# Performance work log

Hardware: AMD Instinct MI355X
Metric: run time of the kernel (lower is better)

## Reference

```python
import jax, jax.numpy as jnp
import numpy as np

B, S, H = 2, 2048, 1024
NH, HD = 16, 64  # num heads, head dim


def setup_inputs() -> dict:
    key = jax.random.key(0)
    ks = jax.random.split(key, 8)
    scale = 0.02
    return {
        "hidden_states": jax.random.normal(ks[0], (B, S, H), dtype=jnp.float32),
        "attention_mask": jnp.zeros((B, 1, 1, S), dtype=jnp.float32),
        "Wq": jax.random.normal(ks[1], (H, H), dtype=jnp.float32) * scale,
        "bq": jnp.zeros((H,), dtype=jnp.float32),
        "Wk": jax.random.normal(ks[2], (H, H), dtype=jnp.float32) * scale,
        "bk": jnp.zeros((H,), dtype=jnp.float32),
        "Wv": jax.random.normal(ks[3], (H, H), dtype=jnp.float32) * scale,
        "bv": jnp.zeros((H,), dtype=jnp.float32),
    }


def _split_heads(x):
    # [B,S,H] -> [B,NH,S,HD]
    b, s, _ = x.shape
    return x.reshape(b, s, NH, HD).transpose(0, 2, 1, 3)


def reference(hidden_states, attention_mask, Wq, bq, Wk, bk, Wv, bv):
    q = _split_heads(hidden_states @ Wq.T + bq)
    k = _split_heads(hidden_states @ Wk.T + bk)
    v = _split_heads(hidden_states @ Wv.T + bv)
    # scores: [B,NH,S,S]
    scores = jnp.einsum("bhqd,bhkd->bhqk", q, k) / jnp.sqrt(jnp.float32(HD))
    scores = scores + attention_mask
    att = jax.nn.softmax(scores, axis=-1)  # dropout is identity in eval
    ctx = jnp.einsum("bhqk,bhkd->bhqd", att, v)
    # [B,NH,S,HD] -> [B,S,H]
    return ctx.transpose(0, 2, 1, 3).reshape(hidden_states.shape[0], hidden_states.shape[1], NH * HD)
```

## Files before the change

kernel.cpp:

```cpp
#include <hip/hip_runtime.h>
#include <stdint.h>

#define BB 2
#define SS 2048
#define HH 1024
#define NH 16
#define HD 64

#define LOG2E 1.4426950408889634f
#define QSCALE (0.125f * LOG2E)

typedef short bfrag  __attribute__((ext_vector_type(8)));
typedef short bfrag4 __attribute__((ext_vector_type(4)));
typedef float f32x4  __attribute__((ext_vector_type(4)));

__device__ __forceinline__ short f2bf(float f) {
    union { float f; uint32_t u; } v; v.f = f;
    uint32_t r = (v.u + 0x7fffu + ((v.u >> 16) & 1u)) >> 16;
    return (short)r;
}

__global__ __launch_bounds__(256) void cvt_all(
    const float* __restrict__ X,  const float* __restrict__ Wq,
    const float* __restrict__ Wk, const float* __restrict__ Wv,
    const float* __restrict__ mask,
    short* __restrict__ Xb, short* __restrict__ Wcat,
    float* __restrict__ maskl)
{
    int i = blockIdx.x * 256 + threadIdx.x;
    if (i >= 1835008) {
        int off = i - 1835008;
        float4 f = ((const float4*)mask)[off];
        f.x *= LOG2E; f.y *= LOG2E; f.z *= LOG2E; f.w *= LOG2E;
        ((float4*)maskl)[off] = f;
        return;
    }
    const float* src; short* dst; int off;
    if (i < 1048576)      { src = X;  dst = Xb;                 off = i; }
    else if (i < 1310720) { src = Wq; dst = Wcat;               off = i - 1048576; }
    else if (i < 1572864) { src = Wk; dst = Wcat + 1048576;     off = i - 1310720; }
    else                  { src = Wv; dst = Wcat + 2097152;     off = i - 1572864; }
    float4 f = ((const float4*)src)[off];
    short4 s;
    s.x = f2bf(f.x); s.y = f2bf(f.y); s.z = f2bf(f.z); s.w = f2bf(f.w);
    ((short4*)dst)[off] = s;
}

__device__ __forceinline__ void gload_lds16(const void* g, void* lds) {
    __builtin_amdgcn_global_load_lds(
        (__attribute__((address_space(1))) void*)(uintptr_t)g,
        (__attribute__((address_space(3))) void*)(uintptr_t)lds,
        16, 0, 0);
}

__global__ __launch_bounds__(256, 3) void qkv_gemm(
    const short* __restrict__ X, const short* __restrict__ Wcat,
    const float* __restrict__ bq, const float* __restrict__ bk, const float* __restrict__ bv,
    short* __restrict__ Qo, short* __restrict__ Ko, short* __restrict__ Vo)
{
    __shared__ __align__(16) short smem[17408];

    const int tid  = threadIdx.x;
    const int wave = tid >> 6, lane = tid & 63;
    const int quad = lane >> 4, l15 = lane & 15;
    const int mTile = blockIdx.y * 128;
    const int nTile = blockIdx.x * 128;
    const int z = nTile >> 10;
    const int nLocT = nTile & 1023;
    const float* bias = (z == 0) ? bq : (z == 1) ? bk : bv;

    f32x4 acc[4][4];
#pragma unroll
    for (int i = 0; i < 4; ++i)
#pragma unroll
        for (int j = 0; j < 4; ++j) acc[i][j] = (f32x4)0.0f;

    const int srow  = lane >> 3;
    const int c_lin = lane & 7;
    const int mBase = (wave >> 1) * 64;
    const int nBase = (wave & 1) * 64;

    for (int k0 = 0; k0 < 1024; k0 += 64) {
        __syncthreads();
#pragma unroll
        for (int i = 0; i < 4; ++i) {
            int row = i * 32 + wave * 8 + srow;
            int cg  = c_lin ^ (row & 7);
            gload_lds16(X + (size_t)(mTile + row) * 1024 + k0 + cg * 8,
                        (char*)smem + i * 4096 + wave * 1024);
            gload_lds16(Wcat + (size_t)(nTile + row) * 1024 + k0 + cg * 8,
                        (char*)smem + 16384 + i * 4096 + wave * 1024);
        }
        __syncthreads();

#pragma unroll
        for (int kt = 0; kt < 2; ++kt) {
            bfrag af[4], bf[4];
#pragma unroll
            for (int t = 0; t < 4; ++t) {
                int arow = mBase + t * 16 + l15;
                int aslot = (kt * 4 + quad) ^ (arow & 7);
                af[t] = *(const bfrag*)((const char*)smem + arow * 128 + aslot * 16);
                int brow = nBase + t * 16 + l15;
                int bslot = (kt * 4 + quad) ^ (brow & 7);
                bf[t] = *(const bfrag*)((const char*)smem + 16384 + brow * 128 + bslot * 16);
            }
#pragma unroll
            for (int mt = 0; mt < 4; ++mt)
#pragma unroll
                for (int ct = 0; ct < 4; ++ct)
                    acc[mt][ct] = __builtin_amdgcn_mfma_f32_16x16x32_bf16(
                        af[mt], bf[ct], acc[mt][ct], 0, 0, 0);
        }
    }

    __syncthreads();
    const int b = mTile >> 11, sBase = mTile & 2047;

    if (z == 2) {
#pragma unroll
        for (int mt = 0; mt < 4; ++mt)
#pragma unroll
            for (int ct = 0; ct < 4; ++ct)
#pragma unroll
                for (int r = 0; r < 4; ++r) {
                    int nl = nBase + ct * 16 + l15;
                    int sl = mBase + mt * 16 + quad * 4 + r;
                    smem[nl * 136 + sl] = f2bf(acc[mt][ct][r] + bias[nLocT + nl]);
                }
        __syncthreads();
#pragma unroll
        for (int p = 0; p < 8; ++p) {
            int nl = p * 16 + (tid >> 4);
            int c  = tid & 15;
            bfrag v8 = *(const bfrag*)(smem + nl * 136 + c * 8);
            int ng = nLocT + nl, hh = ng >> 6, d = ng & 63;
            *(bfrag*)(Vo + ((size_t)(b * 16 + hh) * 64 + d) * 2048 + sBase + c * 8) = v8;
        }
    } else {
        short* Out = (z == 0) ? Qo : Ko;
        float scale = (z == 0) ? QSCALE : 1.0f;
#pragma unroll
        for (int mt = 0; mt < 4; ++mt)
#pragma unroll
            for (int ct = 0; ct < 4; ++ct)
#pragma unroll
                for (int r = 0; r < 4; ++r) {
                    int ml = mBase + mt * 16 + quad * 4 + r;
                    int nl = nBase + ct * 16 + l15;
                    smem[ml * 136 + nl] = f2bf((acc[mt][ct][r] + bias[nLocT + nl]) * scale);
                }
        __syncthreads();
#pragma unroll
        for (int p = 0; p < 8; ++p) {
            int ml = p * 16 + (tid >> 4);
            int c  = tid & 15;
            bfrag v8 = *(const bfrag*)(smem + ml * 136 + c * 8);
            int s  = sBase + ml;
            int nl = nLocT + c * 8, hh = nl >> 6, d = nl & 63;
            *(bfrag*)(Out + (((size_t)(b * 16 + hh) << 11) + s) * 64 + d) = v8;
        }
    }
}

__global__ __launch_bounds__(256, 4) void attn_kernel(
    const short* __restrict__ Qb, const short* __restrict__ Kb, const short* __restrict__ Vb,
    const float* __restrict__ maskl, float* __restrict__ out)
{
    __shared__ __align__(16) char smem[32768];

    const int tid  = threadIdx.x;
    const int wave = tid >> 6, lane = tid & 63;
    const int quad = lane >> 4, l15 = lane & 15;
    const int bh = blockIdx.y, b = bh >> 4, h = bh & 15;
    const int qBase = blockIdx.x * 64 + wave * 16;

    int ksrc[2], vsrc[2];
#pragma unroll
    for (int i = 0; i < 2; ++i) {
        int ci = wave * 128 + i * 64 + lane;
        int r = ci >> 3, c = ci & 7;
        int cs = (c ^ (r & 7)) * 16;
        ksrc[i] = r * 128  + cs;
        vsrc[i] = r * 4096 + cs;
    }
    const char* kPtr = (const char*)(Kb + (size_t)bh * SS * HD);
    const char* vPtr = (const char*)(Vb + (size_t)bh * HD * SS);
    const char* mSrc = (const char*)(maskl + b * SS) + quad * 16;

    const short* Qp = Qb + ((size_t)bh * SS + qBase) * HD;
    bfrag qf[2];
#pragma unroll
    for (int kt = 0; kt < 2; ++kt)
        qf[kt] = *(const bfrag*)(Qp + (size_t)l15 * HD + kt * 32 + quad * 8);

    int kAddr[2];
#pragma unroll
    for (int kt = 0; kt < 2; ++kt)
        kAddr[kt] = l15 * 128 + (((kt * 4 + quad) ^ (l15 & 7)) * 16);
    int vAddr[4];
#pragma unroll
    for (int ct = 0; ct < 4; ++ct)
        vAddr[ct] = 8192 + l15 * 128 + (((ct * 2 + (quad >> 1)) ^ (l15 & 7)) * 16) + (quad & 1) * 8;

    const f32x4 z4 = (f32x4)0.0f;
    const bfrag4 ones = {0x3F80, 0x3F80, 0x3F80, 0x3F80};

    f32x4 oacc[4], ol = z4;
#pragma unroll
    for (int dt = 0; dt < 4; ++dt) oacc[dt] = z4;

#pragma unroll
    for (int i = 0; i < 2; ++i) {
        gload_lds16(kPtr + ksrc[i], smem + wave * 2048 + i * 1024);
        gload_lds16(vPtr + vsrc[i], smem + 8192 + wave * 2048 + i * 1024);
    }
    kPtr += 8192; vPtr += 128;

    for (int j = 0; j < 32; ++j) {
        const int cur = (j & 1) << 14;
        __syncthreads();
        if (j < 31) {
            const int nxt = 16384 - cur;
#pragma unroll
            for (int i = 0; i < 2; ++i) {
                gload_lds16(kPtr + ksrc[i], smem + nxt + wave * 2048 + i * 1024);
                gload_lds16(vPtr + vsrc[i], smem + nxt + 8192 + wave * 2048 + i * 1024);
            }
            kPtr += 8192; vPtr += 128;
        }
        const char* base = smem + cur;

        f32x4 mvl[4];
#pragma unroll
        for (int ct = 0; ct < 4; ++ct)
            mvl[ct] = *(const f32x4*)(mSrc + ct * 64);
        mSrc += 256;

        f32x4 s[4];
#pragma unroll
        for (int ct = 0; ct < 4; ++ct) {
            bfrag kf0 = *(const bfrag*)(base + kAddr[0] + ct * 2048);
            bfrag kf1 = *(const bfrag*)(base + kAddr[1] + ct * 2048);
            s[ct] = __builtin_amdgcn_mfma_f32_16x16x32_bf16(kf0, qf[0], z4,    0, 0, 0);
            s[ct] = __builtin_amdgcn_mfma_f32_16x16x32_bf16(kf1, qf[1], s[ct], 0, 0, 0);
        }

        bfrag4 pf[4];
#pragma unroll
        for (int ct = 0; ct < 4; ++ct) {
            uint32_t a0 = __float_as_uint(exp2f(s[ct][0] + mvl[ct][0])) + 0x8000u;
            uint32_t a1 = __float_as_uint(exp2f(s[ct][1] + mvl[ct][1])) + 0x8000u;
            uint32_t a2 = __float_as_uint(exp2f(s[ct][2] + mvl[ct][2])) + 0x8000u;
            uint32_t a3 = __float_as_uint(exp2f(s[ct][3] + mvl[ct][3])) + 0x8000u;
            union { uint32_t u[2]; bfrag4 v; } cvt;
            cvt.u[0] = __builtin_amdgcn_perm(a1, a0, 0x07060302u);
            cvt.u[1] = __builtin_amdgcn_perm(a3, a2, 0x07060302u);
            pf[ct] = cvt.v;
        }

#pragma unroll
        for (int dt = 0; dt < 4; ++dt) {
#pragma unroll
            for (int ct = 0; ct < 4; ++ct) {
                bfrag4 vf = *(const bfrag4*)(base + vAddr[ct] + dt * 2048);
                oacc[dt] = __builtin_amdgcn_mfma_f32_16x16x16bf16_1k(pf[ct], vf, oacc[dt], 0, 0, 0);
            }
        }
#pragma unroll
        for (int ct = 0; ct < 4; ++ct)
            ol = __builtin_amdgcn_mfma_f32_16x16x16bf16_1k(pf[ct], ones, ol, 0, 0, 0);
    }

#pragma unroll
    for (int r = 0; r < 4; ++r) {
        float linv = 1.0f / ol[r];
        int qrow = qBase + quad * 4 + r;
#pragma unroll
        for (int dt = 0; dt < 4; ++dt)
            out[((size_t)(b * SS + qrow)) * HH + h * 64 + dt * 16 + l15] =
                oacc[dt][r] * linv;
    }
}

extern "C" void kernel_launch(void* const* d_in, const int* in_sizes, int n_in,
                              void* d_out, int out_size, void* d_ws, size_t ws_size,
                              hipStream_t stream) {
    const float* hs   = (const float*)d_in[0];
    const float* mask = (const float*)d_in[1];
    const float* Wq   = (const float*)d_in[2];
    const float* bq   = (const float*)d_in[3];
    const float* Wk   = (const float*)d_in[4];
    const float* bk   = (const float*)d_in[5];
    const float* Wv   = (const float*)d_in[6];
    const float* bv   = (const float*)d_in[7];
    float* out = (float*)d_out;

    char* ws = (char*)d_ws;
    short* Xb    = (short*)(ws);
    short* Wcat  = (short*)(ws + (8ull  << 20));
    short* Qb    = (short*)(ws + (14ull << 20));
    short* Kb    = (short*)(ws + (22ull << 20));
    short* Vb    = (short*)(ws + (30ull << 20));
    float* maskl = (float*)(ws + (38ull << 20));

    cvt_all<<<7172, 256, 0, stream>>>(hs, Wq, Wk, Wv, mask, Xb, Wcat, maskl);

    qkv_gemm<<<dim3(24, 32), 256, 0, stream>>>(Xb, Wcat, bq, bk, bv, Qb, Kb, Vb);

    attn_kernel<<<dim3(SS / 64, BB * NH), 256, 0, stream>>>(Qb, Kb, Vb, maskl, out);
}
```

Baseline: 184.7 us.

## Have each attention wave process 32 query rows with two waves per block

The attention block shrinks from four waves to two, and each wave now handles two 16-row query halves. Every K and V fragment read from LDS then feeds two MFMA chains, which halves the LDS traffic per unit of compute. Each wave loads four chunks per tile to keep the K/V staging per block unchanged. In exchange, registers per wave and the work per wave both grow, and there are fewer waves per block to hide latency. The launch-bounds occupancy hint also drops to 2.

```diff
diff --git a/kernel.cpp b/kernel.cpp
--- a/kernel.cpp
+++ b/kernel.cpp
@@ -163,7 +163,7 @@
     }
 }
 
-__global__ __launch_bounds__(256, 4) void attn_kernel(
+__global__ __launch_bounds__(128, 2) void attn_kernel(
     const short* __restrict__ Qb, const short* __restrict__ Kb, const short* __restrict__ Vb,
     const float* __restrict__ maskl, float* __restrict__ out)
 {
@@ -173,12 +173,12 @@
     const int wave = tid >> 6, lane = tid & 63;
     const int quad = lane >> 4, l15 = lane & 15;
     const int bh = blockIdx.y, b = bh >> 4, h = bh & 15;
-    const int qBase = blockIdx.x * 64 + wave * 16;
-
-    int ksrc[2], vsrc[2];
-#pragma unroll
-    for (int i = 0; i < 2; ++i) {
-        int ci = wave * 128 + i * 64 + lane;
+    const int qBase = blockIdx.x * 64 + wave * 32;
+
+    int ksrc[4], vsrc[4];
+#pragma unroll
+    for (int i = 0; i < 4; ++i) {
+        int ci = wave * 256 + i * 64 + lane;
         int r = ci >> 3, c = ci & 7;
         int cs = (c ^ (r & 7)) * 16;
         ksrc[i] = r * 128  + cs;
@@ -189,10 +189,12 @@
     const char* mSrc = (const char*)(maskl + b * SS) + quad * 16;
 
     const short* Qp = Qb + ((size_t)bh * SS + qBase) * HD;
-    bfrag qf[2];
-#pragma unroll
-    for (int kt = 0; kt < 2; ++kt)
-        qf[kt] = *(const bfrag*)(Qp + (size_t)l15 * HD + kt * 32 + quad * 8);
+    bfrag qf[2][2];
+#pragma unroll
+    for (int hf = 0; hf < 2; ++hf)
+#pragma unroll
+        for (int kt = 0; kt < 2; ++kt)
+            qf[hf][kt] = *(const bfrag*)(Qp + (size_t)(hf * 16 + l15) * HD + kt * 32 + quad * 8);
 
     int kAddr[2];
 #pragma unroll
@@ -206,14 +208,18 @@
     const f32x4 z4 = (f32x4)0.0f;
     const bfrag4 ones = {0x3F80, 0x3F80, 0x3F80, 0x3F80};
 
-    f32x4 oacc[4], ol = z4;
-#pragma unroll
-    for (int dt = 0; dt < 4; ++dt) oacc[dt] = z4;
-
-#pragma unroll
-    for (int i = 0; i < 2; ++i) {
-        gload_lds16(kPtr + ksrc[i], smem + wave * 2048 + i * 1024);
-        gload_lds16(vPtr + vsrc[i], smem + 8192 + wave * 2048 + i * 1024);
+    f32x4 oacc[2][4], ol[2];
+#pragma unroll
+    for (int hf = 0; hf < 2; ++hf) {
+        ol[hf] = z4;
+#pragma unroll
+        for (int dt = 0; dt < 4; ++dt) oacc[hf][dt] = z4;
+    }
+
+#pragma unroll
+    for (int i = 0; i < 4; ++i) {
+        gload_lds16(kPtr + ksrc[i], smem + wave * 4096 + i * 1024);
+        gload_lds16(vPtr + vsrc[i], smem + 8192 + wave * 4096 + i * 1024);
     }
     kPtr += 8192; vPtr += 128;
 
@@ -223,9 +229,9 @@
         if (j < 31) {
             const int nxt = 16384 - cur;
 #pragma unroll
-            for (int i = 0; i < 2; ++i) {
-                gload_lds16(kPtr + ksrc[i], smem + nxt + wave * 2048 + i * 1024);
-                gload_lds16(vPtr + vsrc[i], smem + nxt + 8192 + wave * 2048 + i * 1024);
+            for (int i = 0; i < 4; ++i) {
+                gload_lds16(kPtr + ksrc[i], smem + nxt + wave * 4096 + i * 1024);
+                gload_lds16(vPtr + vsrc[i], smem + nxt + 8192 + wave * 4096 + i * 1024);
             }
             kPtr += 8192; vPtr += 128;
         }
@@ -237,26 +243,36 @@
             mvl[ct] = *(const f32x4*)(mSrc + ct * 64);
         mSrc += 256;
 
-        f32x4 s[4];
+        f32x4 s0[4], s1[4];
 #pragma unroll
         for (int ct = 0; ct < 4; ++ct) {
             bfrag kf0 = *(const bfrag*)(base + kAddr[0] + ct * 2048);
             bfrag kf1 = *(const bfrag*)(base + kAddr[1] + ct * 2048);
-            s[ct] = __builtin_amdgcn_mfma_f32_16x16x32_bf16(kf0, qf[0], z4,    0, 0, 0);
-            s[ct] = __builtin_amdgcn_mfma_f32_16x16x32_bf16(kf1, qf[1], s[ct], 0, 0, 0);
-        }
-
-        bfrag4 pf[4];
+            s0[ct] = __builtin_amdgcn_mfma_f32_16x16x32_bf16(kf0, qf[0][0], z4,     0, 0, 0);
+            s0[ct] = __builtin_amdgcn_mfma_f32_16x16x32_bf16(kf1, qf[0][1], s0[ct], 0, 0, 0);
+            s1[ct] = __builtin_amdgcn_mfma_f32_16x16x32_bf16(kf0, qf[1][0], z4,     0, 0, 0);
+            s1[ct] = __builtin_amdgcn_mfma_f32_16x16x32_bf16(kf1, qf[1][1], s1[ct], 0, 0, 0);
+        }
+
+        bfrag4 pf0[4], pf1[4];
 #pragma unroll
         for (int ct = 0; ct < 4; ++ct) {
-            uint32_t a0 = __float_as_uint(exp2f(s[ct][0] + mvl[ct][0])) + 0x8000u;
-            uint32_t a1 = __float_as_uint(exp2f(s[ct][1] + mvl[ct][1])) + 0x8000u;
-            uint32_t a2 = __float_as_uint(exp2f(s[ct][2] + mvl[ct][2])) + 0x8000u;
-            uint32_t a3 = __float_as_uint(exp2f(s[ct][3] + mvl[ct][3])) + 0x8000u;
             union { uint32_t u[2]; bfrag4 v; } cvt;
+            uint32_t a0, a1, a2, a3;
+            a0 = __float_as_uint(exp2f(s0[ct][0] + mvl[ct][0])) + 0x8000u;
+            a1 = __float_as_uint(exp2f(s0[ct][1] + mvl[ct][1])) + 0x8000u;
+            a2 = __float_as_uint(exp2f(s0[ct][2] + mvl[ct][2])) + 0x8000u;
+            a3 = __float_as_uint(exp2f(s0[ct][3] + mvl[ct][3])) + 0x8000u;
             cvt.u[0] = __builtin_amdgcn_perm(a1, a0, 0x07060302u);
             cvt.u[1] = __builtin_amdgcn_perm(a3, a2, 0x07060302u);
-            pf[ct] = cvt.v;
+            pf0[ct] = cvt.v;
+            a0 = __float_as_uint(exp2f(s1[ct][0] + mvl[ct][0])) + 0x8000u;
+            a1 = __float_as_uint(exp2f(s1[ct][1] + mvl[ct][1])) + 0x8000u;
+            a2 = __float_as_uint(exp2f(s1[ct][2] + mvl[ct][2])) + 0x8000u;
+            a3 = __float_as_uint(exp2f(s1[ct][3] + mvl[ct][3])) + 0x8000u;
+            cvt.u[0] = __builtin_amdgcn_perm(a1, a0, 0x07060302u);
+            cvt.u[1] = __builtin_amdgcn_perm(a3, a2, 0x07060302u);
+            pf1[ct] = cvt.v;
         }
 
 #pragma unroll
@@ -264,22 +280,28 @@
 #pragma unroll
             for (int ct = 0; ct < 4; ++ct) {
                 bfrag4 vf = *(const bfrag4*)(base + vAddr[ct] + dt * 2048);
-                oacc[dt] = __builtin_amdgcn_mfma_f32_16x16x16bf16_1k(pf[ct], vf, oacc[dt], 0, 0, 0);
+                oacc[0][dt] = __builtin_amdgcn_mfma_f32_16x16x16bf16_1k(pf0[ct], vf, oacc[0][dt], 0, 0, 0);
+                oacc[1][dt] = __builtin_amdgcn_mfma_f32_16x16x16bf16_1k(pf1[ct], vf, oacc[1][dt], 0, 0, 0);
             }
         }
 #pragma unroll
-        for (int ct = 0; ct < 4; ++ct)
-            ol = __builtin_amdgcn_mfma_f32_16x16x16bf16_1k(pf[ct], ones, ol, 0, 0, 0);
-    }
-
-#pragma unroll
-    for (int r = 0; r < 4; ++r) {
-        float linv = 1.0f / ol[r];
-        int qrow = qBase + quad * 4 + r;
-#pragma unroll
-        for (int dt = 0; dt < 4; ++dt)
-            out[((size_t)(b * SS + qrow)) * HH + h * 64 + dt * 16 + l15] =
-                oacc[dt][r] * linv;
+        for (int ct = 0; ct < 4; ++ct) {
+            ol[0] = __builtin_amdgcn_mfma_f32_16x16x16bf16_1k(pf0[ct], ones, ol[0], 0, 0, 0);
+            ol[1] = __builtin_amdgcn_mfma_f32_16x16x16bf16_1k(pf1[ct], ones, ol[1], 0, 0, 0);
+        }
+    }
+
+#pragma unroll
+    for (int hf = 0; hf < 2; ++hf) {
+#pragma unroll
+        for (int r = 0; r < 4; ++r) {
+            float linv = 1.0f / ol[hf][r];
+            int qrow = qBase + hf * 16 + quad * 4 + r;
+#pragma unroll
+            for (int dt = 0; dt < 4; ++dt)
+                out[((size_t)(b * SS + qrow)) * HH + h * 64 + dt * 16 + l15] =
+                    oacc[hf][dt][r] * linv;
+        }
     }
 }
 
@@ -308,5 +330,5 @@
 
     qkv_gemm<<<dim3(24, 32), 256, 0, stream>>>(Xb, Wcat, bq, bk, bv, Qb, Kb, Vb);
 
-    attn_kernel<<<dim3(SS / 64, BB * NH), 256, 0, stream>>>(Qb, Kb, Vb, maskl, out);
-}
+    attn_kernel<<<dim3(SS / 64, BB * NH), 128, 0, stream>>>(Qb, Kb, Vb, maskl, out);
+}
```

Result: slower. 201.9 us (+9.3%).
